# Performance work log

Measured on AMD Instinct MI355X. Metric: run time of the kernel, lower is better.

Reference implementation:

```python
import jax, jax.numpy as jnp
import numpy as np

N_NODES = 100000
N_EDGES = 1600000
IN_CH = 128
OUT_CH = 64
HID = 2 * OUT_CH  # 128


def setup_inputs() -> dict:
    key = jax.random.key(0)
    ks = jax.random.split(key, 8)
    s = lambda fan_in: 1.0 / np.sqrt(fan_in)
    return {
        "x": jax.random.normal(ks[0], (N_NODES, IN_CH), jnp.float32),
        "edge_index": jax.random.randint(ks[1], (2, N_EDGES), 0, N_NODES, dtype=jnp.int32),
        "W1": jax.random.normal(ks[2], (IN_CH, HID), jnp.float32) * s(IN_CH),
        "b1": jnp.zeros((HID,), jnp.float32),
        "W2": jax.random.normal(ks[3], (HID, HID), jnp.float32) * s(HID),
        "b2": jnp.zeros((HID,), jnp.float32),
        "W3": jax.random.normal(ks[4], (HID, OUT_CH), jnp.float32) * s(HID),
        "b3": jnp.zeros((OUT_CH,), jnp.float32),
    }


def reference(x, edge_index, W1, b1, W2, b2, W3, b3):
    N = x.shape[0]
    # GCNConv (PyG semantics): add self-loops, symmetric deg^{-1/2} normalization,
    # linear transform, scatter-add aggregation at destination, then bias.
    loops = jnp.arange(N, dtype=edge_index.dtype)
    src = jnp.concatenate([edge_index[0], loops])  # [E+N]
    dst = jnp.concatenate([edge_index[1], loops])  # [E+N]
    deg = jnp.zeros((N,), x.dtype).at[dst].add(1.0)  # in-degree incl. self-loop
    dinv = jnp.where(deg > 0, jax.lax.rsqrt(deg), 0.0)
    norm = (dinv[src] * dinv[dst])[:, None]  # [E+N, 1]

    def gcn_conv(h, W, b):
        h = h @ W  # transform first (smaller when out < in)
        msg = h[src] * norm  # gather + normalize, [E+N, C]
        agg = jnp.zeros((N, h.shape[1]), h.dtype).at[dst].add(msg)  # scatter-add
        return agg + b

    h = jax.nn.relu(gcn_conv(x, W1, b1))
    h = jax.nn.relu(gcn_conv(h, W2, b2))
    h = gcn_conv(h, W3, b3)
    return jnp.min(h, axis=0)  # min-pool over nodes -> [OUT_CH]
```

## Files before the change

kernel.cpp:

```cpp
#include <hip/hip_runtime.h>
#include <stdint.h>
#include <stddef.h>
#include <float.h>

typedef short bf16x8 __attribute__((ext_vector_type(8)));
typedef float f32x4 __attribute__((ext_vector_type(4)));

#define NB 256

static __device__ __forceinline__ unsigned enc_min(float v) {
  unsigned u = __float_as_uint(v);
  return (u & 0x80000000u) ? ~u : (u | 0x80000000u);
}
static __device__ __forceinline__ unsigned short f2bf(float f) {
  unsigned u = __float_as_uint(f);
  u += 0x7fffu + ((u >> 16) & 1u);
  return (unsigned short)(u >> 16);
}
static __device__ __forceinline__ float bf2f(unsigned short b) {
  return __uint_as_float(((unsigned)b) << 16);
}
static __device__ __forceinline__ void acc8(float* a, uint4 v) {
  a[0] += __uint_as_float(v.x << 16);
  a[1] += __uint_as_float(v.x & 0xffff0000u);
  a[2] += __uint_as_float(v.y << 16);
  a[3] += __uint_as_float(v.y & 0xffff0000u);
  a[4] += __uint_as_float(v.z << 16);
  a[5] += __uint_as_float(v.z & 0xffff0000u);
  a[6] += __uint_as_float(v.w << 16);
  a[7] += __uint_as_float(v.w & 0xffff0000u);
}

__global__ __launch_bounds__(256) void k_binA(const int* __restrict__ edge, int E,
                                              int* __restrict__ bin_cur,
                                              int2* __restrict__ pairs,
                                              int binw, int bcap) {
  __shared__ int h[NB], gbase[NB];
  int tid = threadIdx.x;
  int base = blockIdx.x * 4096;
  h[tid] = 0;
  if (tid + 0 == tid) {}
  __syncthreads();
  int d_[16], s_[16], pk[16];
#pragma unroll
  for (int k = 0; k < 16; ++k) {
    int e = base + k * 256 + tid;
    d_[k] = -1;
    if (e < E) {
      int d = edge[E + e];
      int s = edge[e];
      int g = (int)((unsigned)d / (unsigned)binw);
      int rk = atomicAdd(&h[g], 1);
      pk[k] = (g << 16) | rk;
      d_[k] = d;
      s_[k] = s;
    }
  }
  __syncthreads();
  if (h[tid] > 0) gbase[tid] = atomicAdd(&bin_cur[tid * 16], h[tid]);
  __syncthreads();
#pragma unroll
  for (int k = 0; k < 16; ++k) {
    if (d_[k] >= 0) {
      int g = pk[k] >> 16;
      int rk = pk[k] & 0xffff;
      int p = gbase[g] + rk;
      if (p < bcap) pairs[(size_t)g * bcap + p] = make_int2(d_[k], s_[k]);
    }
  }
}

__global__ void k_scanB(const int* __restrict__ bin_cur, int* __restrict__ bucket_base) {
  __shared__ int sm[NB];
  int tid = threadIdx.x;
  int v = bin_cur[tid * 16];
  sm[tid] = v;
  __syncthreads();
  for (int off = 1; off < NB; off <<= 1) {
    int t = (tid >= off) ? sm[tid - off] : 0;
    __syncthreads();
    sm[tid] += t;
    __syncthreads();
  }
  bucket_base[tid] = sm[tid] - v;
}

__global__ __launch_bounds__(256) void k_buildB(const int2* __restrict__ pairs,
                                                const int* __restrict__ bin_cur,
                                                const int* __restrict__ bucket_base,
                                                int bcap, int binw, int N, int E,
                                                int* __restrict__ row_ptr,
                                                float* __restrict__ dinv,
                                                int* __restrict__ srcs) {
  __shared__ int cnt_s[512], cur_s[512], sm[512];
  int tid = threadIdx.x;
  int b = blockIdx.x;
  int d0 = b * binw;
  int dcnt = N - d0;
  if (dcnt > binw) dcnt = binw;
  if (dcnt < 0) dcnt = 0;
  int nb_e = bin_cur[b * 16];
  if (nb_e > bcap) nb_e = bcap;
  int bbase = bucket_base[b];
  const int2* pp = pairs + (size_t)b * bcap;

  cnt_s[tid] = 0;
  cnt_s[tid + 256] = 0;
  __syncthreads();
  for (int i = tid; i < nb_e; i += 256) {
    int2 pr = pp[i];
    atomicAdd(&cnt_s[pr.x - d0], 1);
  }
  __syncthreads();
  int c0 = cnt_s[tid], c1 = cnt_s[tid + 256];
  sm[tid] = c0;
  sm[tid + 256] = c1;
  __syncthreads();
  for (int off = 1; off < 512; off <<= 1) {
    int t0 = (tid >= off) ? sm[tid - off] : 0;
    int i1 = tid + 256;
    int t1 = (i1 >= off) ? sm[i1 - off] : 0;
    __syncthreads();
    sm[tid] += t0;
    sm[i1] += t1;
    __syncthreads();
  }
  int e0 = sm[tid] - c0, e1 = sm[tid + 256] - c1;
  if (tid < dcnt) {
    row_ptr[d0 + tid] = bbase + e0;
    dinv[d0 + tid] = 1.0f / sqrtf((float)(c0 + 1));
  }
  if (tid + 256 < dcnt) {
    row_ptr[d0 + tid + 256] = bbase + e1;
    dinv[d0 + tid + 256] = 1.0f / sqrtf((float)(c1 + 1));
  }
  cur_s[tid] = e0;
  cur_s[tid + 256] = e1;
  if (tid == 0 && d0 + dcnt == N) row_ptr[N] = E;
  __syncthreads();
  for (int i = tid; i < nb_e; i += 256) {
    int2 pr = pp[i];
    int slot = bbase + atomicAdd(&cur_s[pr.x - d0], 1);
    srcs[slot] = pr.y;
  }
}

__global__ void k_prepw(const float* __restrict__ W1, const float* __restrict__ W2,
                        const float* __restrict__ W3,
                        unsigned short* __restrict__ w1h, unsigned short* __restrict__ w1l,
                        unsigned short* __restrict__ w2h, unsigned short* __restrict__ w2l,
                        unsigned short* __restrict__ w3h, unsigned short* __restrict__ w3l) {
  const int K = 128;
  int idx = blockIdx.x * 256 + threadIdx.x;
  const float* W;
  unsigned short *oh, *ol;
  int Nn, base;
  if (idx < 16384) { W = W1; Nn = 128; oh = w1h; ol = w1l; base = idx; }
  else if (idx < 32768) { W = W2; Nn = 128; oh = w2h; ol = w2l; base = idx - 16384; }
  else if (idx < 40960) { W = W3; Nn = 64; oh = w3h; ol = w3l; base = idx - 32768; }
  else return;
  int n = base / K, k = base % K;
  float w = W[(size_t)k * Nn + n];
  unsigned short h = f2bf(w);
  unsigned short l = f2bf(w - bf2f(h));
  int nf = n >> 4, mloc = n & 15, kci = k >> 5, quad = (k >> 3) & 3, j = k & 7;
  size_t o = ((size_t)((nf * 4 + kci) * 64 + quad * 16 + mloc)) * 8 + j;
  oh[o] = h;
  ol[o] = l;
}

template <int NFW>
static __device__ __forceinline__ void gemm_body(const float* __restrict__ A,
                                                 const unsigned short* __restrict__ Wfh,
                                                 const unsigned short* __restrict__ Wfl,
                                                 const float* __restrict__ dinv,
                                                 unsigned short* __restrict__ P, int M,
                                                 int blk) {
  const int K = 128;
  const int COUT = NFW * 64;
  __shared__ unsigned short Ah[64][136];
  __shared__ unsigned short Al[64][136];
  int tid = threadIdx.x;
  int m0 = blk * 64;
  int w = tid >> 6, lane = tid & 63;

  bf16x8 bh[NFW][4], bl[NFW][4];
#pragma unroll
  for (int i = 0; i < NFW; ++i)
#pragma unroll
    for (int kci = 0; kci < 4; ++kci) {
      size_t o = ((size_t)(((w * NFW + i) * 4 + kci) * 64 + lane)) * 8;
      bh[i][kci] = *(const bf16x8*)&Wfh[o];
      bl[i][kci] = *(const bf16x8*)&Wfl[o];
    }

#pragma unroll
  for (int q = 0; q < 8; ++q) {
    int f = q * 256 + tid;
    int m = f >> 5, k4 = f & 31;
    int row = m0 + m;
    if (row >= M) row = M - 1;
    float4 v = *(const float4*)&A[(size_t)row * K + k4 * 4];
    unsigned short h0 = f2bf(v.x), h1 = f2bf(v.y), h2 = f2bf(v.z), h3 = f2bf(v.w);
    unsigned short l0 = f2bf(v.x - bf2f(h0)), l1 = f2bf(v.y - bf2f(h1));
    unsigned short l2 = f2bf(v.z - bf2f(h2)), l3 = f2bf(v.w - bf2f(h3));
    uint2 hh, ll;
    hh.x = (unsigned)h0 | ((unsigned)h1 << 16);
    hh.y = (unsigned)h2 | ((unsigned)h3 << 16);
    ll.x = (unsigned)l0 | ((unsigned)l1 << 16);
    ll.y = (unsigned)l2 | ((unsigned)l3 << 16);
    *(uint2*)&Ah[m][k4 * 4] = hh;
    *(uint2*)&Al[m][k4 * 4] = ll;
  }
  __syncthreads();

  int mloc = lane & 15, quad = lane >> 4;
  f32x4 acc[4][NFW];
#pragma unroll
  for (int rt = 0; rt < 4; ++rt)
#pragma unroll
    for (int i = 0; i < NFW; ++i) acc[rt][i] = (f32x4){0.f, 0.f, 0.f, 0.f};

#pragma unroll
  for (int rt = 0; rt < 4; ++rt) {
    const unsigned short* ph = &Ah[rt * 16 + mloc][quad * 8];
    const unsigned short* pl = &Al[rt * 16 + mloc][quad * 8];
#pragma unroll
    for (int kci = 0; kci < 4; ++kci) {
      bf16x8 ah = *(const bf16x8*)(ph + kci * 32);
      bf16x8 al = *(const bf16x8*)(pl + kci * 32);
#pragma unroll
      for (int i = 0; i < NFW; ++i) {
        acc[rt][i] = __builtin_amdgcn_mfma_f32_16x16x32_bf16(al, bh[i][kci], acc[rt][i], 0, 0, 0);
        acc[rt][i] = __builtin_amdgcn_mfma_f32_16x16x32_bf16(ah, bl[i][kci], acc[rt][i], 0, 0, 0);
        acc[rt][i] = __builtin_amdgcn_mfma_f32_16x16x32_bf16(ah, bh[i][kci], acc[rt][i], 0, 0, 0);
      }
    }
  }

#pragma unroll
  for (int rt = 0; rt < 4; ++rt) {
    int rbase = m0 + rt * 16 + quad * 4;
#pragma unroll
    for (int r = 0; r < 4; ++r) {
      int row = rbase + r;
      if (row < M) {
        float dv = dinv[row];
#pragma unroll
        for (int i = 0; i < NFW; ++i) {
          int nf = w * NFW + i;
          P[(size_t)row * COUT + nf * 16 + mloc] = f2bf(acc[rt][i][r] * dv);
        }
      }
    }
  }
}

__global__ __launch_bounds__(256) void k_gemm1(const float* __restrict__ A,
                                               const unsigned short* __restrict__ Wfh,
                                               const unsigned short* __restrict__ Wfl,
                                               const float* __restrict__ dinv,
                                               unsigned short* __restrict__ P, int M) {
  gemm_body<2>(A, Wfh, Wfl, dinv, P, M, blockIdx.x);
}

template <int NFW>
__global__ __launch_bounds__(256) void k_agg_gemm(const unsigned short* __restrict__ Pin,
                                                  const int* __restrict__ row_ptr,
                                                  const int* __restrict__ srcs,
                                                  const float* __restrict__ dinv,
                                                  const float* __restrict__ bias,
                                                  const unsigned short* __restrict__ Wfh,
                                                  const unsigned short* __restrict__ Wfl,
                                                  unsigned short* __restrict__ Pout, int N) {
  const int COUT = NFW * 64;
  __shared__ unsigned short Ah[16][136];
  __shared__ unsigned short Al[16][136];
  int tid = threadIdx.x;
  int wv = tid >> 6, lane = tid & 63;
  int grp = lane >> 4, sub = lane & 15;
  int m = wv * 4 + grp;
  int d = blockIdx.x * 16 + m;
  int dc = d < N ? d : N - 1;
  bool valid = d < N;
  unsigned soff = (unsigned)sub * 16u;
  const char* Pb = (const char*)Pin;

  float a[8] = {0.f, 0.f, 0.f, 0.f, 0.f, 0.f, 0.f, 0.f};
  {
    uint4 v = *(const uint4*)(Pb + ((unsigned)dc * 256u + soff));
    acc8(a, v);
  }
  int lo = row_ptr[dc];
  int hi = row_ptr[valid ? d + 1 : dc];
  int j = lo;
  for (; j + 8 <= hi; j += 8) {
    unsigned id[8];
    uint4 vv[8];
#pragma unroll
    for (int k = 0; k < 8; ++k) id[k] = (unsigned)srcs[j + k];
#pragma unroll
    for (int k = 0; k < 8; ++k) vv[k] = *(const uint4*)(Pb + (id[k] * 256u + soff));
#pragma unroll
    for (int k = 0; k < 8; ++k) acc8(a, vv[k]);
  }
  for (; j + 4 <= hi; j += 4) {
    unsigned id[4];
    uint4 vv[4];
#pragma unroll
    for (int k = 0; k < 4; ++k) id[k] = (unsigned)srcs[j + k];
#pragma unroll
    for (int k = 0; k < 4; ++k) vv[k] = *(const uint4*)(Pb + (id[k] * 256u + soff));
#pragma unroll
    for (int k = 0; k < 4; ++k) acc8(a, vv[k]);
  }
  for (; j < hi; ++j) {
    unsigned i0 = (unsigned)srcs[j];
    uint4 v0 = *(const uint4*)(Pb + (i0 * 256u + soff));
    acc8(a, v0);
  }

  bf16x8 bh[NFW][4], bl[NFW][4];
#pragma unroll
  for (int i = 0; i < NFW; ++i)
#pragma unroll
    for (int kci = 0; kci < 4; ++kci) {
      size_t o = ((size_t)(((wv * NFW + i) * 4 + kci) * 64 + lane)) * 8;
      bh[i][kci] = *(const bf16x8*)&Wfh[o];
      bl[i][kci] = *(const bf16x8*)&Wfl[o];
    }

  float dv = dinv[dc];
  int ch0 = sub * 8;
  float4 bv0 = *(const float4*)&bias[ch0];
  float4 bv1 = *(const float4*)&bias[ch0 + 4];
  float h[8];
  h[0] = dv * a[0] + bv0.x; h[1] = dv * a[1] + bv0.y;
  h[2] = dv * a[2] + bv0.z; h[3] = dv * a[3] + bv0.w;
  h[4] = dv * a[4] + bv1.x; h[5] = dv * a[5] + bv1.y;
  h[6] = dv * a[6] + bv1.z; h[7] = dv * a[7] + bv1.w;
#pragma unroll
  for (int k = 0; k < 8; ++k) h[k] = fmaxf(h[k], 0.f);
  unsigned short hb[8], lb[8];
#pragma unroll
  for (int k = 0; k < 8; ++k) {
    hb[k] = f2bf(h[k]);
    lb[k] = f2bf(h[k] - bf2f(hb[k]));
  }
  uint4 HH, LL;
  HH.x = (unsigned)hb[0] | ((unsigned)hb[1] << 16);
  HH.y = (unsigned)hb[2] | ((unsigned)hb[3] << 16);
  HH.z = (unsigned)hb[4] | ((unsigned)hb[5] << 16);
  HH.w = (unsigned)hb[6] | ((unsigned)hb[7] << 16);
  LL.x = (unsigned)lb[0] | ((unsigned)lb[1] << 16);
  LL.y = (unsigned)lb[2] | ((unsigned)lb[3] << 16);
  LL.z = (unsigned)lb[4] | ((unsigned)lb[5] << 16);
  LL.w = (unsigned)lb[6] | ((unsigned)lb[7] << 16);
  *(uint4*)&Ah[m][ch0] = HH;
  *(uint4*)&Al[m][ch0] = LL;
  __syncthreads();

  int mloc = lane & 15, quad = lane >> 4;
  f32x4 acc[NFW];
#pragma unroll
  for (int i = 0; i < NFW; ++i) acc[i] = (f32x4){0.f, 0.f, 0.f, 0.f};
#pragma unroll
  for (int kci = 0; kci < 4; ++kci) {
    bf16x8 ah = *(const bf16x8*)&Ah[mloc][quad * 8 + kci * 32];
    bf16x8 al = *(const bf16x8*)&Al[mloc][quad * 8 + kci * 32];
#pragma unroll
    for (int i = 0; i < NFW; ++i) {
      acc[i] = __builtin_amdgcn_mfma_f32_16x16x32_bf16(al, bh[i][kci], acc[i], 0, 0, 0);
      acc[i] = __builtin_amdgcn_mfma_f32_16x16x32_bf16(ah, bl[i][kci], acc[i], 0, 0, 0);
      acc[i] = __builtin_amdgcn_mfma_f32_16x16x32_bf16(ah, bh[i][kci], acc[i], 0, 0, 0);
    }
  }
  int rbase = blockIdx.x * 16 + quad * 4;
#pragma unroll
  for (int r = 0; r < 4; ++r) {
    int row = rbase + r;
    if (row < N) {
      float dvr = dinv[row];
#pragma unroll
      for (int i = 0; i < NFW; ++i) {
        int nf = wv * NFW + i;
        Pout[(size_t)row * COUT + nf * 16 + mloc] = f2bf(acc[i][r] * dvr);
      }
    }
  }
}

__global__ __launch_bounds__(256) void k_agg_pool(const unsigned short* __restrict__ P,
                                                  const int* __restrict__ row_ptr,
                                                  const int* __restrict__ srcs,
                                                  const float* __restrict__ dinv,
                                                  const float* __restrict__ bias,
                                                  unsigned* __restrict__ minenc, int N) {
  const int CAP = 448;
  __shared__ int s_idx[4][CAP];
  __shared__ float s_red[4][32];
  int tid = threadIdx.x;
  int wv = tid >> 6, lane = tid & 63;
  int b8 = blockIdx.x & 7;
  int slice = b8 >> 2, part = b8 & 3;
  int g0 = ((blockIdx.x >> 3) * 4 + part) * 64 + wv * 16;
  const char* Pb = (const char*)P + slice * 64;

  int i = lane >> 2, q = lane & 3;
  unsigned qoff = (unsigned)q * 16u;
  int d = g0 + i;
  int dc = d < N ? d : N - 1;
  bool valid = d < N;

  int e0 = row_ptr[g0 < N ? g0 : N];
  int e1 = row_ptr[(g0 + 16) < N ? (g0 + 16) : N];
  int lo_n = row_ptr[dc];
  int hi_n = row_ptr[valid ? d + 1 : dc];

  float a[8];
  {
    uint4 v = *(const uint4*)(Pb + ((unsigned)dc * 128u + qoff));
    a[0] = __uint_as_float(v.x << 16);
    a[1] = __uint_as_float(v.x & 0xffff0000u);
    a[2] = __uint_as_float(v.y << 16);
    a[3] = __uint_as_float(v.y & 0xffff0000u);
    a[4] = __uint_as_float(v.z << 16);
    a[5] = __uint_as_float(v.z & 0xffff0000u);
    a[6] = __uint_as_float(v.w << 16);
    a[7] = __uint_as_float(v.w & 0xffff0000u);
  }

  for (int w0 = e0; w0 < e1; w0 += CAP) {
    int wend = min(w0 + CAP, e1);
    int cnt = wend - w0;
    __builtin_amdgcn_wave_barrier();
    for (int t = lane; t < cnt; t += 64) s_idx[wv][t] = srcs[w0 + t];
    __builtin_amdgcn_wave_barrier();
    int j = max(lo_n, w0), hi = min(hi_n, wend);
    for (; j + 4 <= hi; j += 4) {
      unsigned i0 = (unsigned)s_idx[wv][j - w0];
      unsigned i1 = (unsigned)s_idx[wv][j - w0 + 1];
      unsigned i2 = (unsigned)s_idx[wv][j - w0 + 2];
      unsigned i3 = (unsigned)s_idx[wv][j - w0 + 3];
      uint4 v0 = *(const uint4*)(Pb + (i0 * 128u + qoff));
      uint4 v1 = *(const uint4*)(Pb + (i1 * 128u + qoff));
      uint4 v2 = *(const uint4*)(Pb + (i2 * 128u + qoff));
      uint4 v3 = *(const uint4*)(Pb + (i3 * 128u + qoff));
      acc8(a, v0);
      acc8(a, v1);
      acc8(a, v2);
      acc8(a, v3);
    }
    for (; j < hi; ++j) {
      unsigned i0 = (unsigned)s_idx[wv][j - w0];
      uint4 v0 = *(const uint4*)(Pb + (i0 * 128u + qoff));
      acc8(a, v0);
    }
  }

  int c0 = slice * 32 + q * 8;
  float dv = dinv[dc];
  float4 bv0 = *(const float4*)&bias[c0];
  float4 bv1 = *(const float4*)&bias[c0 + 4];
  float h[8];
  h[0] = dv * a[0] + bv0.x; h[1] = dv * a[1] + bv0.y;
  h[2] = dv * a[2] + bv0.z; h[3] = dv * a[3] + bv0.w;
  h[4] = dv * a[4] + bv1.x; h[5] = dv * a[5] + bv1.y;
  h[6] = dv * a[6] + bv1.z; h[7] = dv * a[7] + bv1.w;

  if (!valid) {
#pragma unroll
    for (int k = 0; k < 8; ++k) h[k] = FLT_MAX;
  }
#pragma unroll
  for (int off = 4; off < 64; off <<= 1) {
#pragma unroll
    for (int k = 0; k < 8; ++k) h[k] = fminf(h[k], __shfl_xor(h[k], off, 64));
  }
  if (lane < 4) {
#pragma unroll
    for (int k = 0; k < 8; ++k) s_red[wv][q * 8 + k] = h[k];
  }
  __syncthreads();
  if (tid < 32) {
    float mn = fminf(fminf(s_red[0][tid], s_red[1][tid]),
                     fminf(s_red[2][tid], s_red[3][tid]));
    atomicMin(&minenc[slice * 32 + tid], enc_min(mn));
  }
}

__global__ void k_decode(const unsigned* __restrict__ minenc, float* __restrict__ out) {
  int c = threadIdx.x;
  unsigned k = minenc[c];
  unsigned u = (k & 0x80000000u) ? (k & 0x7FFFFFFFu) : ~k;
  out[c] = __uint_as_float(u);
}

extern "C" void kernel_launch(void* const* d_in, const int* in_sizes, int n_in,
                              void* d_out, int out_size, void* d_ws, size_t ws_size,
                              hipStream_t stream) {
  const float* X  = (const float*)d_in[0];
  const int* edge = (const int*)d_in[1];
  const float* W1 = (const float*)d_in[2];
  const float* b1 = (const float*)d_in[3];
  const float* W2 = (const float*)d_in[4];
  const float* b2 = (const float*)d_in[5];
  const float* W3 = (const float*)d_in[6];
  const float* b3 = (const float*)d_in[7];
  float* out = (float*)d_out;

  const int IN_CH = 128;
  int N = in_sizes[0] / IN_CH;
  int E = in_sizes[1] / 2;

  char* ws = (char*)d_ws;
  size_t off = 0;
  auto alloc = [&](size_t bytes) {
    void* p = ws + off;
    off = (off + bytes + 255) & ~(size_t)255;
    return p;
  };
  unsigned short* P1 = (unsigned short*)alloc((size_t)N * 128 * 2);
  unsigned short* P2 = (unsigned short*)alloc((size_t)N * 128 * 2);
  int* srcs      = (int*)alloc((size_t)E * 4);
  int* row_ptr   = (int*)alloc((size_t)(N + 1) * 4);
  float* dinv    = (float*)alloc((size_t)N * 4);
  int* bin_cur   = (int*)alloc((size_t)NB * 16 * 4);
  int* bucket_base = (int*)alloc((size_t)NB * 4);
  unsigned* minenc = (unsigned*)alloc(256);
  unsigned short* w1h = (unsigned short*)alloc(16384 * 2);
  unsigned short* w1l = (unsigned short*)alloc(16384 * 2);
  unsigned short* w2h = (unsigned short*)alloc(16384 * 2);
  unsigned short* w2l = (unsigned short*)alloc(16384 * 2);
  unsigned short* w3h = (unsigned short*)alloc(8192 * 2);
  unsigned short* w3l = (unsigned short*)alloc(8192 * 2);

  int binw = (N + NB - 1) / NB;
  int bcap = E / NB + 1024;
  int2* pairs = (int2*)P2;
  unsigned short* P3 = P1;

  hipMemsetAsync(bin_cur, 0, (size_t)NB * 16 * 4, stream);
  hipMemsetAsync(minenc, 0xFF, 64 * 4, stream);

  int gx = (N + 63) / 64;
  int nta = (E + 4095) / 4096;
  int gagg = (N + 15) / 16;
  int c64 = (N + 255) / 256;
  k_prepw<<<160, 256, 0, stream>>>(W1, W2, W3, w1h, w1l, w2h, w2l, w3h, w3l);
  k_binA<<<nta, 256, 0, stream>>>(edge, E, bin_cur, pairs, binw, bcap);
  k_scanB<<<1, NB, 0, stream>>>(bin_cur, bucket_base);
  k_buildB<<<NB, 256, 0, stream>>>(pairs, bin_cur, bucket_base, bcap, binw, N, E,
                                   row_ptr, dinv, srcs);
  k_gemm1<<<gx, 256, 0, stream>>>(X, w1h, w1l, dinv, P1, N);
  k_agg_gemm<2><<<gagg, 256, 0, stream>>>(P1, row_ptr, srcs, dinv, b1, w2h, w2l, P2, N);
  k_agg_gemm<1><<<gagg, 256, 0, stream>>>(P2, row_ptr, srcs, dinv, b2, w3h, w3l, P3, N);
  k_agg_pool<<<c64 * 8, 256, 0, stream>>>(P3, row_ptr, srcs, dinv, b3, minenc, N);
  k_decode<<<1, 64, 0, stream>>>(minenc, out);
}
```

Before: 362.7 us.

## Merge preprocessing kernels and overlap CSR scatter with first GEMM

Folds the weight-prep kernel into the binning kernel as extra blocks, and folds the bucket scan into each build block. It also splits the CSR build so the source-index scatter runs as extra blocks of the first GEMM launch. This drops the launch count from five to three and lets the scatter overlap with GEMM work. In exchange, every build block now repeats the 256-entry scan, and the pairs buffer is read twice across two kernels.

Result: faster. 355.5 us (-2.0%).

```diff
diff --git a/kernel.cpp b/kernel.cpp
--- a/kernel.cpp
+++ b/kernel.cpp
@@ -31,15 +31,43 @@
   a[7] += __uint_as_float(v.w & 0xffff0000u);
 }
 
-__global__ __launch_bounds__(256) void k_binA(const int* __restrict__ edge, int E,
-                                              int* __restrict__ bin_cur,
-                                              int2* __restrict__ pairs,
-                                              int binw, int bcap) {
+__global__ __launch_bounds__(256) void k_bin_prep(const int* __restrict__ edge, int E,
+                                                  int* __restrict__ bin_cur,
+                                                  int2* __restrict__ pairs,
+                                                  int binw, int bcap, int nta,
+                                                  const float* __restrict__ W1,
+                                                  const float* __restrict__ W2,
+                                                  const float* __restrict__ W3,
+                                                  unsigned short* __restrict__ w1h,
+                                                  unsigned short* __restrict__ w1l,
+                                                  unsigned short* __restrict__ w2h,
+                                                  unsigned short* __restrict__ w2l,
+                                                  unsigned short* __restrict__ w3h,
+                                                  unsigned short* __restrict__ w3l) {
+  int tid = threadIdx.x;
+  if ((int)blockIdx.x >= nta) {
+    const int K = 128;
+    int idx = ((int)blockIdx.x - nta) * 256 + tid;
+    const float* W;
+    unsigned short *oh, *ol;
+    int Nn, base;
+    if (idx < 16384) { W = W1; Nn = 128; oh = w1h; ol = w1l; base = idx; }
+    else if (idx < 32768) { W = W2; Nn = 128; oh = w2h; ol = w2l; base = idx - 16384; }
+    else if (idx < 40960) { W = W3; Nn = 64; oh = w3h; ol = w3l; base = idx - 32768; }
+    else return;
+    int n = base / K, k = base % K;
+    float w = W[(size_t)k * Nn + n];
+    unsigned short h = f2bf(w);
+    unsigned short l = f2bf(w - bf2f(h));
+    int nf = n >> 4, mloc = n & 15, kci = k >> 5, quad = (k >> 3) & 3, j = k & 7;
+    size_t o = ((size_t)((nf * 4 + kci) * 64 + quad * 16 + mloc)) * 8 + j;
+    oh[o] = h;
+    ol[o] = l;
+    return;
+  }
   __shared__ int h[NB], gbase[NB];
-  int tid = threadIdx.x;
   int base = blockIdx.x * 4096;
   h[tid] = 0;
-  if (tid + 0 == tid) {}
   __syncthreads();
   int d_[16], s_[16], pk[16];
 #pragma unroll
@@ -70,38 +98,31 @@
   }
 }
 
-__global__ void k_scanB(const int* __restrict__ bin_cur, int* __restrict__ bucket_base) {
-  __shared__ int sm[NB];
-  int tid = threadIdx.x;
-  int v = bin_cur[tid * 16];
-  sm[tid] = v;
-  __syncthreads();
-  for (int off = 1; off < NB; off <<= 1) {
-    int t = (tid >= off) ? sm[tid - off] : 0;
-    __syncthreads();
-    sm[tid] += t;
-    __syncthreads();
-  }
-  bucket_base[tid] = sm[tid] - v;
-}
-
-__global__ __launch_bounds__(256) void k_buildB(const int2* __restrict__ pairs,
-                                                const int* __restrict__ bin_cur,
-                                                const int* __restrict__ bucket_base,
-                                                int bcap, int binw, int N, int E,
-                                                int* __restrict__ row_ptr,
-                                                float* __restrict__ dinv,
-                                                int* __restrict__ srcs) {
-  __shared__ int cnt_s[512], cur_s[512], sm[512];
+__global__ __launch_bounds__(256) void k_buildB1(const int* __restrict__ bin_cur,
+                                                 const int2* __restrict__ pairs,
+                                                 int bcap, int binw, int N, int E,
+                                                 int* __restrict__ row_ptr,
+                                                 float* __restrict__ dinv) {
+  __shared__ int tot[NB];
+  __shared__ int cnt_s[512], sm[512];
   int tid = threadIdx.x;
   int b = blockIdx.x;
+  tot[tid] = bin_cur[tid * 16];
+  __syncthreads();
+  for (int off = 1; off < NB; off <<= 1) {
+    int t = (tid >= off) ? tot[tid - off] : 0;
+    __syncthreads();
+    tot[tid] += t;
+    __syncthreads();
+  }
+  int bbase = (b == 0) ? 0 : tot[b - 1];
+  int nb_e = bin_cur[b * 16];
+  if (nb_e > bcap) nb_e = bcap;
+
   int d0 = b * binw;
   int dcnt = N - d0;
   if (dcnt > binw) dcnt = binw;
   if (dcnt < 0) dcnt = 0;
-  int nb_e = bin_cur[b * 16];
-  if (nb_e > bcap) nb_e = bcap;
-  int bbase = bucket_base[b];
   const int2* pp = pairs + (size_t)b * bcap;
 
   cnt_s[tid] = 0;
@@ -134,39 +155,7 @@
     row_ptr[d0 + tid + 256] = bbase + e1;
     dinv[d0 + tid + 256] = 1.0f / sqrtf((float)(c1 + 1));
   }
-  cur_s[tid] = e0;
-  cur_s[tid + 256] = e1;
   if (tid == 0 && d0 + dcnt == N) row_ptr[N] = E;
-  __syncthreads();
-  for (int i = tid; i < nb_e; i += 256) {
-    int2 pr = pp[i];
-    int slot = bbase + atomicAdd(&cur_s[pr.x - d0], 1);
-    srcs[slot] = pr.y;
-  }
-}
-
-__global__ void k_prepw(const float* __restrict__ W1, const float* __restrict__ W2,
-                        const float* __restrict__ W3,
-                        unsigned short* __restrict__ w1h, unsigned short* __restrict__ w1l,
-                        unsigned short* __restrict__ w2h, unsigned short* __restrict__ w2l,
-                        unsigned short* __restrict__ w3h, unsigned short* __restrict__ w3l) {
-  const int K = 128;
-  int idx = blockIdx.x * 256 + threadIdx.x;
-  const float* W;
-  unsigned short *oh, *ol;
-  int Nn, base;
-  if (idx < 16384) { W = W1; Nn = 128; oh = w1h; ol = w1l; base = idx; }
-  else if (idx < 32768) { W = W2; Nn = 128; oh = w2h; ol = w2l; base = idx - 16384; }
-  else if (idx < 40960) { W = W3; Nn = 64; oh = w3h; ol = w3l; base = idx - 32768; }
-  else return;
-  int n = base / K, k = base % K;
-  float w = W[(size_t)k * Nn + n];
-  unsigned short h = f2bf(w);
-  unsigned short l = f2bf(w - bf2f(h));
-  int nf = n >> 4, mloc = n & 15, kci = k >> 5, quad = (k >> 3) & 3, j = k & 7;
-  size_t o = ((size_t)((nf * 4 + kci) * 64 + quad * 16 + mloc)) * 8 + j;
-  oh[o] = h;
-  ol[o] = l;
 }
 
 template <int NFW>
@@ -256,12 +245,37 @@
   }
 }
 
-__global__ __launch_bounds__(256) void k_gemm1(const float* __restrict__ A,
-                                               const unsigned short* __restrict__ Wfh,
-                                               const unsigned short* __restrict__ Wfl,
-                                               const float* __restrict__ dinv,
-                                               unsigned short* __restrict__ P, int M) {
-  gemm_body<2>(A, Wfh, Wfl, dinv, P, M, blockIdx.x);
+__global__ __launch_bounds__(256) void k_scatter_gemm(const float* __restrict__ A,
+                                                      const unsigned short* __restrict__ Wfh,
+                                                      const unsigned short* __restrict__ Wfl,
+                                                      const float* __restrict__ dinv,
+                                                      unsigned short* __restrict__ P, int M,
+                                                      const int2* __restrict__ pairs,
+                                                      const int* __restrict__ bin_cur, int bcap,
+                                                      const int* __restrict__ row_ptr,
+                                                      int binw, int N,
+                                                      int* __restrict__ srcs) {
+  if ((int)blockIdx.x >= NB) {
+    gemm_body<2>(A, Wfh, Wfl, dinv, P, M, blockIdx.x - NB);
+    return;
+  }
+  __shared__ int cur_s[512];
+  int tid = threadIdx.x;
+  int b = blockIdx.x;
+  int d0 = b * binw;
+  int dcnt = N - d0;
+  if (dcnt > binw) dcnt = binw;
+  if (dcnt < 0) dcnt = 0;
+  int nb_e = bin_cur[b * 16];
+  if (nb_e > bcap) nb_e = bcap;
+  const int2* pp = pairs + (size_t)b * bcap;
+  if (tid < dcnt) cur_s[tid] = row_ptr[d0 + tid];
+  if (tid + 256 < dcnt) cur_s[tid + 256] = row_ptr[d0 + tid + 256];
+  __syncthreads();
+  for (int i = tid; i < nb_e; i += 256) {
+    int2 pr = pp[i];
+    srcs[atomicAdd(&cur_s[pr.x - d0], 1)] = pr.y;
+  }
 }
 
 template <int NFW>
@@ -526,7 +540,6 @@
   int* row_ptr   = (int*)alloc((size_t)(N + 1) * 4);
   float* dinv    = (float*)alloc((size_t)N * 4);
   int* bin_cur   = (int*)alloc((size_t)NB * 16 * 4);
-  int* bucket_base = (int*)alloc((size_t)NB * 4);
   unsigned* minenc = (unsigned*)alloc(256);
   unsigned short* w1h = (unsigned short*)alloc(16384 * 2);
   unsigned short* w1l = (unsigned short*)alloc(16384 * 2);
@@ -547,12 +560,11 @@
   int nta = (E + 4095) / 4096;
   int gagg = (N + 15) / 16;
   int c64 = (N + 255) / 256;
-  k_prepw<<<160, 256, 0, stream>>>(W1, W2, W3, w1h, w1l, w2h, w2l, w3h, w3l);
-  k_binA<<<nta, 256, 0, stream>>>(edge, E, bin_cur, pairs, binw, bcap);
-  k_scanB<<<1, NB, 0, stream>>>(bin_cur, bucket_base);
-  k_buildB<<<NB, 256, 0, stream>>>(pairs, bin_cur, bucket_base, bcap, binw, N, E,
-                                   row_ptr, dinv, srcs);
-  k_gemm1<<<gx, 256, 0, stream>>>(X, w1h, w1l, dinv, P1, N);
+  k_bin_prep<<<nta + 160, 256, 0, stream>>>(edge, E, bin_cur, pairs, binw, bcap, nta,
+                                            W1, W2, W3, w1h, w1l, w2h, w2l, w3h, w3l);
+  k_buildB1<<<NB, 256, 0, stream>>>(bin_cur, pairs, bcap, binw, N, E, row_ptr, dinv);
+  k_scatter_gemm<<<NB + gx, 256, 0, stream>>>(X, w1h, w1l, dinv, P1, N,
+                                              pairs, bin_cur, bcap, row_ptr, binw, N, srcs);
   k_agg_gemm<2><<<gagg, 256, 0, stream>>>(P1, row_ptr, srcs, dinv, b1, w2h, w2l, P2, N);
   k_agg_gemm<1><<<gagg, 256, 0, stream>>>(P2, row_ptr, srcs, dinv, b2, w3h, w3l, P3, N);
   k_agg_pool<<<c64 * 8, 256, 0, stream>>>(P3, row_ptr, srcs, dinv, b3, minenc, N);
```
